# Kernel optimization log

Hardware: AMD Instinct MI355X
Metric: run time of the kernel (lower is better)

## Reference

```python
import jax, jax.numpy as jnp
import numpy as np
from jax import lax

# Key identity used: modulating ALL weights of output channel o by s_o (with no bias
# inside the modulated conv, as in the source where F.conv2d(..., bias=None)) is
# mathematically identical to a plain conv followed by per-(batch, out_channel)
# scaling of the output. This collapses the per-sample Python loop into one conv.

def _upsample2x(x):
    # nearest-neighbor x2, matching F.interpolate(scale_factor=2) default mode
    return jnp.repeat(jnp.repeat(x, 2, axis=2), 2, axis=3)

def _conv(x, w):
    return lax.conv_general_dilated(
        x, w, window_strides=(1, 1), padding=[(1, 1), (1, 1)],
        dimension_numbers=("NCHW", "OIHW", "NCHW"))

def _modconv(x, style, w, fc_w, fc_b):
    # style_fc: [B, style_dim] -> [B, out_ch]
    s = style @ fc_w.T + fc_b          # [B, O]
    y = _conv(x, w)                    # [B, O, H, W]
    return y * s[:, :, None, None]


def setup_inputs() -> dict:
    key = jax.random.key(0)
    ks = jax.random.split(key, 16)
    B, SD = 8, 512
    chans = [(512, 256), (256, 128), (128, 64), (64, 64), (64, 64)]
    inp = {
        "x": jax.random.normal(ks[0], (B, 512, 8, 8), jnp.float32),
        "style": jax.random.normal(ks[1], (B, SD), jnp.float32),
    }
    for i, (ci, co) in enumerate(chans, start=1):
        inp[f"w{i}"] = jax.random.normal(ks[2 * i], (co, ci, 3, 3), jnp.float32) * (1.0 / np.sqrt(ci * 9))
        inp[f"fw{i}"] = jax.random.normal(ks[2 * i + 1], (co, SD), jnp.float32) * (1.0 / np.sqrt(SD))
        inp[f"fb{i}"] = jnp.ones((co,), jnp.float32)
    inp["wf"] = jax.random.normal(ks[12], (3, 64, 3, 3), jnp.float32) * (1.0 / np.sqrt(64 * 9))
    inp["bf"] = jnp.zeros((3,), jnp.float32)
    return inp


def reference(x, style, w1, fw1, fb1, w2, fw2, fb2, w3, fw3, fb3,
              w4, fw4, fb4, w5, fw5, fb5, wf, bf):
    x = _upsample2x(x)
    x = jax.nn.relu(_modconv(x, style, w1, fw1, fb1))
    x = _upsample2x(x)
    x = jax.nn.relu(_modconv(x, style, w2, fw2, fb2))
    x = _upsample2x(x)
    x = jax.nn.relu(_modconv(x, style, w3, fw3, fb3))
    x = _upsample2x(x)
    x = jax.nn.relu(_modconv(x, style, w4, fw4, fb4))
    x = _upsample2x(x)
    x = jax.nn.relu(_modconv(x, style, w5, fw5, fb5))
    x = _conv(x, wf) + bf[None, :, None, None]
    return x
```

## Files before the change

kernel.cpp:

```cpp
#include <hip/hip_runtime.h>
#include <hip/hip_bf16.h>
#include <cstddef>

typedef __bf16 bf16x8 __attribute__((ext_vector_type(8)));
typedef float f32x4 __attribute__((ext_vector_type(4)));

__global__ void prep_all_kernel(const float* __restrict__ x, __hip_bfloat16* __restrict__ act0,
                                const float* __restrict__ w1, __hip_bfloat16* __restrict__ o1,
                                const float* __restrict__ w2, __hip_bfloat16* __restrict__ o2,
                                const float* __restrict__ w3, __hip_bfloat16* __restrict__ o3,
                                const float* __restrict__ w4, __hip_bfloat16* __restrict__ o4,
                                const float* __restrict__ w5, __hip_bfloat16* __restrict__ o5,
                                const float* __restrict__ wf, __hip_bfloat16* __restrict__ of,
                                const float* __restrict__ style,
                                const float* __restrict__ fw1, const float* __restrict__ fb1,
                                const float* __restrict__ fw2, const float* __restrict__ fb2,
                                const float* __restrict__ fw3, const float* __restrict__ fb3,
                                const float* __restrict__ fw4, const float* __restrict__ fb4,
                                const float* __restrict__ fw5, const float* __restrict__ fb5,
                                float* __restrict__ S) {
    const int blk = blockIdx.x;
    if (blk < 1024) {
        int t = blk * 256 + threadIdx.x;
        int c = t & 511; int rest = t >> 9;
        int w = rest & 7; rest >>= 3; int h = rest & 7; int b = rest >> 3;
        act0[t] = __float2bfloat16(x[((b * 512 + c) * 8 + h) * 8 + w]);
    } else if (blk < 12324) {
        int t = (blk - 1024) * 256 + threadIdx.x;
        if (t < 2752512) {
            const float* w; __hip_bfloat16* o; int CI, lgCICH, lgCO16;
            if      (t < 2097152) { w = w1; o = o1; CI = 512; lgCICH = 3; lgCO16 = 4; }
            else if (t < 2621440) { t -= 2097152; w = w2; o = o2; CI = 256; lgCICH = 2; lgCO16 = 3; }
            else                  { t -= 2621440; w = w3; o = o3; CI = 128; lgCICH = 1; lgCO16 = 2; }
            int j    = t & 7;
            int ln   = (t >> 3) & 63;
            int ch   = (t >> 9) & 1;
            int cich = (t >> 10) & ((1 << lgCICH) - 1);
            int co16 = (t >> (10 + lgCICH)) & ((1 << lgCO16) - 1);
            int tap  = (t >> (10 + lgCICH + lgCO16)) & 3;
            int cls  = (t >> (12 + lgCICH + lgCO16)) & 3;
            int co = co16 * 16 + (ln & 15);
            int ci = cich * 64 + ch * 32 + (ln >> 4) * 8 + j;
            int py = cls >> 1, px = cls & 1;
            int i = tap >> 1, jj = tap & 1;
            int r0 = i * (1 + py), rc = py ? (2 - i) : (1 + i);
            int c0 = jj * (1 + px), cc = px ? (2 - jj) : (1 + jj);
            const float* wb = w + ((size_t)co * CI + ci) * 9;
            float s = 0.f;
            for (int rr = 0; rr < rc; ++rr)
                for (int c2 = 0; c2 < cc; ++c2)
                    s += wb[(r0 + rr) * 3 + (c0 + c2)];
            o[t] = __float2bfloat16(s);
        } else if (t < 2883584) {
            int u = t - 2752512;
            const float* w; __hip_bfloat16* o;
            if (u < 65536) { w = w4; o = o4; }
            else           { u -= 65536; w = w5; o = o5; }
            int j   = u & 7;
            int ln  = (u >> 3) & 63;
            int ch  = (u >> 9) & 1;
            int nt  = (u >> 10) & 3;
            int tp  = (u >> 12) & 3;
            int cls = (u >> 14) & 3;
            int py = cls >> 1, px = cls & 1;
            int i = tp >> 1, jj = tp & 1;
            int co = nt * 16 + (ln & 15);
            int ci = ch * 32 + (ln >> 4) * 8 + j;
            int r0 = i * (1 + py), rc = py ? (2 - i) : (1 + i);
            int c0 = jj * (1 + px), cc = px ? (2 - jj) : (1 + jj);
            const float* wb = w + ((size_t)co * 64 + ci) * 9;
            float s = 0.f;
            for (int rr = 0; rr < rc; ++rr)
                for (int c2 = 0; c2 < cc; ++c2)
                    s += wb[(r0 + rr) * 3 + (c0 + c2)];
            o[u] = __float2bfloat16(s);
        } else if (t < 2892800) {
            int u = t - 2883584;
            int j  = u & 7;
            int ln = (u >> 3) & 63;
            int ch = (u >> 9) & 1;
            int tap = u >> 10;
            int rr = ln & 15, qq = ln >> 4;
            int pos = ch * 32 + qq * 8 + j;
            int ci = (pos & 3) * 16 + (pos >> 2);
            float v = (rr < 3) ? wf[((size_t)rr * 64 + ci) * 9 + tap] : 0.f;
            of[u] = __float2bfloat16(v);
        }
    } else {
        int wvid = (blk - 12324) * 4 + (threadIdx.x >> 6);
        int lane = threadIdx.x & 63;
        const float* fw; const float* fb; int lg, sOff, local;
        if      (wvid < 2048) { fw = fw1; fb = fb1; lg = 8; sOff = 0;    local = wvid; }
        else if (wvid < 3072) { fw = fw2; fb = fb2; lg = 7; sOff = 2048; local = wvid - 2048; }
        else if (wvid < 3584) { fw = fw3; fb = fb3; lg = 6; sOff = 3072; local = wvid - 3072; }
        else if (wvid < 4096) { fw = fw4; fb = fb4; lg = 6; sOff = 3584; local = wvid - 3584; }
        else                  { fw = fw5; fb = fb5; lg = 6; sOff = 4096; local = wvid - 4096; }
        int b = local >> lg, o = local & ((1 << lg) - 1);
        const float* sb = style + b * 512;
        const float* fwo = fw + (size_t)o * 512;
        float p = 0.f;
        #pragma unroll
        for (int k = lane; k < 512; k += 64) p += sb[k] * fwo[k];
        #pragma unroll
        for (int off = 32; off > 0; off >>= 1) p += __shfl_down(p, off);
        if (lane == 0) S[sOff + local] = p + fb[o];
    }
}

template <int HS, int CI, int CO, int NT>
__launch_bounds__(256)
__global__ void conv_sfull_kernel(const __hip_bfloat16* __restrict__ actIn,
                                  const __hip_bfloat16* __restrict__ wpk,
                                  const float* __restrict__ S,
                                  __hip_bfloat16* __restrict__ actOut) {
    constexpr int WS = HS, HO = HS * 2;
    constexpr int CICH = CI / 64, CO16 = CO / 16;
    constexpr int PW = HO / 8, PPI = PW * PW;

    const int tid = threadIdx.x;
    const int lane = tid & 63, wv = tid >> 6;
    const int r = lane & 15, q = lane >> 4;
    const int rr2 = r >> 2, cc2 = r & 3;
    const int lane8 = lane * 8;
    const int py = wv >> 1, px = wv & 1;

    const int b = blockIdx.x / PPI;
    const int prest = blockIdx.x - b * PPI;
    const int ph = prest / PW, pwi = prest - ph * PW;
    const int oh0 = ph * 8, ow0 = pwi * 8;
    const int sh0 = oh0 >> 1, sw0 = ow0 >> 1;
    const int co16base = blockIdx.y * NT;
    const int n0 = co16base * 16;

    __shared__ alignas(16) __hip_bfloat16 Tile[36 * 72];

    f32x4 acc[NT];
    #pragma unroll
    for (int j = 0; j < NT; ++j) acc[j] = f32x4{0.f, 0.f, 0.f, 0.f};

    bf16x8 bA[NT][2], bB[NT][2];

    #pragma unroll 1
    for (int cich = 0; cich < CICH; ++cich) {
        if (cich) __syncthreads();
        for (int i = tid; i < 288; i += 256) {
            int pix = i >> 3, koct = i & 7;
            int tr = pix / 6, tc2 = pix - tr * 6;
            int su = sh0 - 1 + tr, sv = sw0 - 1 + tc2;
            uint4 v = {0, 0, 0, 0};
            if (su >= 0 && su < HS && sv >= 0 && sv < WS)
                v = *(const uint4*)(actIn +
                    ((size_t)((b * HS + su) * WS + sv) * CI + cich * 64 + koct * 8));
            *(uint4*)&Tile[pix * 72 + koct * 8] = v;
        }
        __syncthreads();

        auto loadB = [&](bf16x8 (&dst)[NT][2], int tp) {
            #pragma unroll
            for (int nt = 0; nt < NT; ++nt)
                #pragma unroll
                for (int ch = 0; ch < 2; ++ch)
                    dst[nt][ch] = *(const bf16x8*)(wpk +
                        ((size_t)((((wv * 4 + tp) * CO16 + co16base + nt) * CICH + cich) * 2 + ch) << 9) + lane8);
        };

        auto compute = [&](int tp, bf16x8 (&bfr)[NT][2]) {
            const int i = tp >> 1, j = tp & 1;
            const int apix = (rr2 + i + py) * 6 + (cc2 + j + px);
            #pragma unroll
            for (int ch = 0; ch < 2; ++ch) {
                bf16x8 af = *(const bf16x8*)&Tile[apix * 72 + ch * 32 + q * 8];
                #pragma unroll
                for (int nt = 0; nt < NT; ++nt)
                    acc[nt] = __builtin_amdgcn_mfma_f32_16x16x32_bf16(
                        af, bfr[nt][ch], acc[nt], 0, 0, 0);
            }
        };

        loadB(bA, 0);
        loadB(bB, 1);
        compute(0, bA);
        loadB(bA, 2);
        compute(1, bB);
        loadB(bB, 3);
        compute(2, bA);
        compute(3, bB);
    }

    float sv_[NT];
    #pragma unroll
    for (int nt = 0; nt < NT; ++nt) sv_[nt] = S[b * CO + n0 + nt * 16 + r];
    #pragma unroll
    for (int t2 = 0; t2 < 4; ++t2) {
        const int m = q * 4 + t2;
        const int row = oh0 + 2 * (m >> 2) + py;
        const int col = ow0 + 2 * (m & 3) + px;
        const size_t obase = ((size_t)(b * HO + row) * HO + col) * CO + n0;
        #pragma unroll
        for (int nt = 0; nt < NT; ++nt)
            actOut[obase + nt * 16 + r] =
                __float2bfloat16(fmaxf(acc[nt][t2] * sv_[nt], 0.f));
    }
}

template <int HS, int WS>
__launch_bounds__(256)
__global__ void conv_patch_kernel(const __hip_bfloat16* __restrict__ actIn,
                                  const __hip_bfloat16* __restrict__ wpk,
                                  const float* __restrict__ S,
                                  __hip_bfloat16* __restrict__ actOut) {
    constexpr int HO = HS * 2, WO = WS * 2;

    const int tid = threadIdx.x;
    const int lane = tid & 63, wv = tid >> 6;
    const int r = lane & 15, q = lane >> 4;
    const int rs = r >> 3, sc = r & 7;
    const int lane8 = lane * 8;
    const int py = wv >> 1, px = wv & 1;

    const int pw = WO / 16, ppb = (HO / 16) * pw;
    const int b = blockIdx.x / ppb;
    const int prest = blockIdx.x - b * ppb;
    const int ph = prest / pw, pwi = prest - ph * pw;
    const int oh0 = ph * 16, ow0 = pwi * 16;
    const int sh0 = oh0 >> 1, sw0 = ow0 >> 1;

    __shared__ alignas(16) __hip_bfloat16 Tile[100 * 72];

    f32x4 acc[4][4];
    #pragma unroll
    for (int i = 0; i < 4; ++i)
        #pragma unroll
        for (int j = 0; j < 4; ++j) acc[i][j] = f32x4{0.f, 0.f, 0.f, 0.f};

    for (int i = tid; i < 800; i += 256) {
        int pix = i >> 3, koct = i & 7;
        int tr = pix / 10, tc2 = pix - tr * 10;
        int su = sh0 - 1 + tr, sv = sw0 - 1 + tc2;
        uint4 v = {0, 0, 0, 0};
        if (su >= 0 && su < HS && sv >= 0 && sv < WS)
            v = *(const uint4*)(actIn + ((size_t)((b * HS + su) * WS + sv) * 64 + koct * 8));
        *(uint4*)&Tile[pix * 72 + koct * 8] = v;
    }
    __syncthreads();

    const __hip_bfloat16* wcls = wpk + ((size_t)wv << 14);

    bf16x8 bA[4][2], bB[4][2];

    auto loadB = [&](bf16x8 (&dst)[4][2], int tp) {
        #pragma unroll
        for (int nt = 0; nt < 4; ++nt)
            #pragma unroll
            for (int ch = 0; ch < 2; ++ch)
                dst[nt][ch] = *(const bf16x8*)(wcls + (tp << 12) + ((nt * 2 + ch) << 9) + lane8);
    };

    auto compute = [&](int tp, bf16x8 (&bfr)[4][2]) {
        const int i = tp >> 1, j = tp & 1;
        const int ro = i + py, co2 = j + px;
        int apix[4];
        #pragma unroll
        for (int mt = 0; mt < 4; ++mt)
            apix[mt] = (2 * mt + rs + ro) * 10 + (sc + co2);
        #pragma unroll
        for (int ch = 0; ch < 2; ++ch) {
            bf16x8 af[4];
            #pragma unroll
            for (int mt = 0; mt < 4; ++mt)
                af[mt] = *(const bf16x8*)&Tile[apix[mt] * 72 + ch * 32 + q * 8];
            #pragma unroll
            for (int mt = 0; mt < 4; ++mt)
                #pragma unroll
                for (int nt = 0; nt < 4; ++nt)
                    acc[mt][nt] = __builtin_amdgcn_mfma_f32_16x16x32_bf16(
                        af[mt], bfr[nt][ch], acc[mt][nt], 0, 0, 0);
        }
    };

    loadB(bA, 0);
    loadB(bB, 1);
    compute(0, bA);
    loadB(bA, 2);
    compute(1, bB);
    loadB(bB, 3);
    compute(2, bA);
    compute(3, bB);

    float sv_[4];
    #pragma unroll
    for (int nt = 0; nt < 4; ++nt) sv_[nt] = S[b * 64 + nt * 16 + r];
    #pragma unroll
    for (int mt = 0; mt < 4; ++mt) {
        #pragma unroll
        for (int t2 = 0; t2 < 4; ++t2) {
            const int m = q * 4 + t2;
            const int row = oh0 + 4 * mt + 2 * (m >> 3) + py;
            const int col = ow0 + 2 * (m & 7) + px;
            const size_t obase = ((size_t)(b * HO + row) * WO + col) * 64;
            #pragma unroll
            for (int nt = 0; nt < 4; ++nt)
                actOut[obase + nt * 16 + r] =
                    __float2bfloat16(fmaxf(acc[mt][nt][t2] * sv_[nt], 0.f));
        }
    }
}

__launch_bounds__(512)
__global__ void conv_s5f_kernel(const __hip_bfloat16* __restrict__ actIn,
                                const __hip_bfloat16* __restrict__ wpk5,
                                const __hip_bfloat16* __restrict__ wpkF,
                                const float* __restrict__ S,
                                const float* __restrict__ bias,
                                float* __restrict__ out) {
    constexpr int HS = 128, WS = 128;

    const int tid = threadIdx.x;
    const int lane = tid & 63, wv = tid >> 6;
    const int r = lane & 15, q = lane >> 4;
    const int lane8 = lane * 8;
    const int cls = wv >> 1, half = wv & 1;
    const int py = cls >> 1, px = cls & 1;

    const int bid = blockIdx.x;
    const int b = bid >> 8;
    const int rest = bid & 255;
    const int oh0 = (rest >> 4) * 16, ow0 = (rest & 15) * 16;
    const int sh0 = oh0 >> 1, sw0 = ow0 >> 1;

    __shared__ alignas(16) __hip_bfloat16 Lds[18 * 18 * 72];
    __hip_bfloat16* TileA = Lds;

    for (int i = tid; i < 800; i += 512) {
        int pix = i >> 3, koct = i & 7;
        int tr = pix / 10, tc2 = pix - tr * 10;
        int su = sh0 - 1 + tr, sv = sw0 - 1 + tc2;
        uint4 v = {0, 0, 0, 0};
        if (su >= 0 && su < HS && sv >= 0 && sv < WS)
            v = *(const uint4*)(actIn + ((size_t)((b * HS + su) * WS + sv) * 64 + koct * 8));
        *(uint4*)&TileA[pix * 72 + koct * 8] = v;
    }
    __syncthreads();

    f32x4 acc[3][4];
    #pragma unroll
    for (int i = 0; i < 3; ++i)
        #pragma unroll
        for (int j = 0; j < 4; ++j) acc[i][j] = f32x4{0.f, 0.f, 0.f, 0.f};

    int jrA[3], jcA[3];
    #pragma unroll
    for (int mt = 0; mt < 3; ++mt) {
        int pm = half * 48 + mt * 16 + r;
        pm = pm > 80 ? 80 : pm;
        jrA[mt] = (pm * 57) >> 9;
        jcA[mt] = pm - jrA[mt] * 9;
    }

    const __hip_bfloat16* wcls = wpk5 + ((size_t)cls << 14);

    bf16x8 bA[4][2], bB[4][2];

    auto loadB = [&](bf16x8 (&dst)[4][2], int tp) {
        #pragma unroll
        for (int nt = 0; nt < 4; ++nt)
            #pragma unroll
            for (int ch = 0; ch < 2; ++ch)
                dst[nt][ch] = *(const bf16x8*)(wcls + (tp << 12) + ((nt * 2 + ch) << 9) + lane8);
    };

    auto compute = [&](int tp, bf16x8 (&bfr)[4][2]) {
        const int i = tp >> 1, j = tp & 1;
        int apix[3];
        #pragma unroll
        for (int mt = 0; mt < 3; ++mt)
            apix[mt] = (jrA[mt] + i) * 10 + (jcA[mt] + j);
        #pragma unroll
        for (int ch = 0; ch < 2; ++ch) {
            bf16x8 af[3];
            #pragma unroll
            for (int mt = 0; mt < 3; ++mt)
                af[mt] = *(const bf16x8*)&TileA[apix[mt] * 72 + ch * 32 + q * 8];
            #pragma unroll
            for (int mt = 0; mt < 3; ++mt)
                #pragma unroll
                for (int nt = 0; nt < 4; ++nt)
                    acc[mt][nt] = __builtin_amdgcn_mfma_f32_16x16x32_bf16(
                        af[mt], bfr[nt][ch], acc[mt][nt], 0, 0, 0);
        }
    };

    loadB(bA, 0);
    loadB(bB, 1);
    compute(0, bA);
    loadB(bA, 2);
    compute(1, bB);
    loadB(bB, 3);
    compute(2, bA);
    compute(3, bB);

    float sv_[4];
    #pragma unroll
    for (int nt = 0; nt < 4; ++nt) sv_[nt] = S[b * 64 + nt * 16 + r];

    __syncthreads();

    #pragma unroll
    for (int mt = 0; mt < 3; ++mt) {
        #pragma unroll
        for (int t2 = 0; t2 < 4; ++t2) {
            const int m = half * 48 + mt * 16 + q * 4 + t2;
            if (m < 81) {
                const int jr = (m * 57) >> 9;
                const int jc = m - jr * 9;
                const int p  = py ? (oh0 - 1 + 2 * jr) : (oh0 + 2 * jr);
                const int pc = px ? (ow0 - 1 + 2 * jc) : (ow0 + 2 * jc);
                const bool valid = (p >= 0) && (p < 256) && (pc >= 0) && (pc < 256);
                const int dpx = (2 * jr + 1 - py) * 18 + (2 * jc + 1 - px);
                union { ushort4 u; __hip_bfloat16 h[4]; } pk;
                #pragma unroll
                for (int nt = 0; nt < 4; ++nt) {
                    float v = valid ? fmaxf(acc[mt][nt][t2] * sv_[nt], 0.f) : 0.f;
                    pk.h[nt] = __float2bfloat16(v);
                }
                *(ushort4*)&Lds[dpx * 72 + r * 4] = pk.u;
            }
        }
    }
    __syncthreads();

    f32x4 acc2[2];
    acc2[0] = f32x4{0.f, 0.f, 0.f, 0.f};
    acc2[1] = f32x4{0.f, 0.f, 0.f, 0.f};

    #pragma unroll 1
    for (int tap = 0; tap < 9; ++tap) {
        const int dyv = tap / 3;
        const int dxv = tap - dyv * 3;
        const int tc = r + dxv;
        int apix[2];
        #pragma unroll
        for (int mt = 0; mt < 2; ++mt)
            apix[mt] = (wv * 2 + mt + dyv) * 18 + tc;
        #pragma unroll
        for (int ch = 0; ch < 2; ++ch) {
            bf16x8 bfr = *(const bf16x8*)(wpkF + ((tap * 2 + ch) << 9) + lane8);
            #pragma unroll
            for (int mt = 0; mt < 2; ++mt) {
                bf16x8 af = *(const bf16x8*)&Lds[apix[mt] * 72 + ch * 32 + q * 8];
                acc2[mt] = __builtin_amdgcn_mfma_f32_16x16x32_bf16(af, bfr, acc2[mt], 0, 0, 0);
            }
        }
    }

    if (r < 3) {
        const float bs = bias[r];
        #pragma unroll
        for (int mt = 0; mt < 2; ++mt) {
            const int prow = oh0 + wv * 2 + mt;
            #pragma unroll
            for (int t2 = 0; t2 < 4; ++t2)
                out[((size_t)(b * 3 + r) << 16) + prow * 256 + ow0 + q * 4 + t2] =
                    acc2[mt][t2] + bs;
        }
    }
}

extern "C" void kernel_launch(void* const* d_in, const int* in_sizes, int n_in,
                              void* d_out, int out_size, void* d_ws, size_t ws_size,
                              hipStream_t stream) {
    const float* x    = (const float*)d_in[0];
    const float* sty  = (const float*)d_in[1];
    const float* w1   = (const float*)d_in[2];
    const float* fw1  = (const float*)d_in[3];
    const float* fb1  = (const float*)d_in[4];
    const float* w2   = (const float*)d_in[5];
    const float* fw2  = (const float*)d_in[6];
    const float* fb2  = (const float*)d_in[7];
    const float* w3   = (const float*)d_in[8];
    const float* fw3  = (const float*)d_in[9];
    const float* fb3  = (const float*)d_in[10];
    const float* w4   = (const float*)d_in[11];
    const float* fw4  = (const float*)d_in[12];
    const float* fb4  = (const float*)d_in[13];
    const float* w5   = (const float*)d_in[14];
    const float* fw5  = (const float*)d_in[15];
    const float* fb5  = (const float*)d_in[16];
    const float* wf   = (const float*)d_in[17];
    const float* bf   = (const float*)d_in[18];
    float* out = (float*)d_out;

    char* ws = (char*)d_ws;
    size_t off = 0;
    auto alloc = [&](size_t bytes) {
        char* p = ws + off;
        off += (bytes + 255) & ~(size_t)255;
        return p;
    };
    float* S1 = (float*)alloc(8 * 256 * 4);
    float* S2 = (float*)alloc(8 * 128 * 4);
    float* S3 = (float*)alloc(8 * 64 * 4);
    float* S4 = (float*)alloc(8 * 64 * 4);
    float* S5 = (float*)alloc(8 * 64 * 4);
    __hip_bfloat16* act0 = (__hip_bfloat16*)alloc((size_t)262144 * 2);
    __hip_bfloat16* act1 = (__hip_bfloat16*)alloc((size_t)524288 * 2);
    __hip_bfloat16* act2 = (__hip_bfloat16*)alloc((size_t)1048576 * 2);
    __hip_bfloat16* act3 = (__hip_bfloat16*)alloc((size_t)2097152 * 2);
    __hip_bfloat16* act4 = (__hip_bfloat16*)alloc((size_t)8388608 * 2);
    __hip_bfloat16* wt1  = (__hip_bfloat16*)alloc((size_t)2097152 * 2);
    __hip_bfloat16* wt2  = (__hip_bfloat16*)alloc((size_t)524288 * 2);
    __hip_bfloat16* wt3  = (__hip_bfloat16*)alloc((size_t)131072 * 2);
    __hip_bfloat16* wt4  = (__hip_bfloat16*)alloc((size_t)65536 * 2);
    __hip_bfloat16* wt5  = (__hip_bfloat16*)alloc((size_t)65536 * 2);
    __hip_bfloat16* wtF  = (__hip_bfloat16*)alloc((size_t)9 * 16 * 64 * 2);
    if (off > ws_size) return;

    prep_all_kernel<<<13476, 256, 0, stream>>>(x, act0,
                                               w1, wt1, w2, wt2, w3, wt3,
                                               w4, wt4, w5, wt5, wf, wtF,
                                               sty, fw1, fb1, fw2, fb2, fw3, fb3,
                                               fw4, fb4, fw5, fb5, S1);

    conv_sfull_kernel<8, 512, 256, 1><<<dim3(32, 16), 256, 0, stream>>>(act0, wt1, S1, act1);
    conv_sfull_kernel<16, 256, 128, 2><<<dim3(128, 4), 256, 0, stream>>>(act1, wt2, S2, act2);
    conv_sfull_kernel<32, 128, 64, 4><<<dim3(512, 1), 256, 0, stream>>>(act2, wt3, S3, act3);

    conv_patch_kernel<64, 64><<<dim3(512), 256, 0, stream>>>(act3, wt4, S4, act4);

    conv_s5f_kernel<<<2048, 512, 0, stream>>>(act4, wt5, wtF, S5, bf, out);
}
```

Baseline: 194.0 us.

## Fuse stage-4 conv into stage-5/final kernel, recomputing stage-4 tiles with halo

Layer 4's upsample-conv is folded into the combined layer-5 and final-conv kernel. Each block loads a 7x7 stage-3 patch, computes the 10x10 stage-4 tile with its halo in LDS, then runs layers 5 and final as before. This drops the 16 MB act4 write and read round trip and one kernel launch. In exchange, the halo regions of layer 4 are recomputed in neighbouring blocks, and each block uses more LDS. The layer-5 weight packing now permutes input channels to match the LDS layout that the fused stage writes.

```diff
diff --git a/kernel.cpp b/kernel.cpp
--- a/kernel.cpp
+++ b/kernel.cpp
@@ -53,9 +53,9 @@
             o[t] = __float2bfloat16(s);
         } else if (t < 2883584) {
             int u = t - 2752512;
-            const float* w; __hip_bfloat16* o;
-            if (u < 65536) { w = w4; o = o4; }
-            else           { u -= 65536; w = w5; o = o5; }
+            const float* w; __hip_bfloat16* o; bool perm;
+            if (u < 65536) { w = w4; o = o4; perm = false; }
+            else           { u -= 65536; w = w5; o = o5; perm = true; }
             int j   = u & 7;
             int ln  = (u >> 3) & 63;
             int ch  = (u >> 9) & 1;
@@ -65,7 +65,8 @@
             int py = cls >> 1, px = cls & 1;
             int i = tp >> 1, jj = tp & 1;
             int co = nt * 16 + (ln & 15);
-            int ci = ch * 32 + (ln >> 4) * 8 + j;
+            int pos = ch * 32 + (ln >> 4) * 8 + j;
+            int ci = perm ? ((pos & 3) * 16 + (pos >> 2)) : pos;
             int r0 = i * (1 + py), rc = py ? (2 - i) : (1 + i);
             int c0 = jj * (1 + px), cc = px ? (2 - jj) : (1 + jj);
             const float* wb = w + ((size_t)co * 64 + ci) * 9;
@@ -203,49 +204,125 @@
     }
 }
 
-template <int HS, int WS>
-__launch_bounds__(256)
-__global__ void conv_patch_kernel(const __hip_bfloat16* __restrict__ actIn,
-                                  const __hip_bfloat16* __restrict__ wpk,
-                                  const float* __restrict__ S,
-                                  __hip_bfloat16* __restrict__ actOut) {
-    constexpr int HO = HS * 2, WO = WS * 2;
-
+__launch_bounds__(512)
+__global__ void conv_s45f_kernel(const __hip_bfloat16* __restrict__ actIn,
+                                 const __hip_bfloat16* __restrict__ wpk4,
+                                 const __hip_bfloat16* __restrict__ wpk5,
+                                 const __hip_bfloat16* __restrict__ wpkF,
+                                 const float* __restrict__ S4,
+                                 const float* __restrict__ S5,
+                                 const float* __restrict__ bias,
+                                 float* __restrict__ out) {
     const int tid = threadIdx.x;
     const int lane = tid & 63, wv = tid >> 6;
     const int r = lane & 15, q = lane >> 4;
-    const int rs = r >> 3, sc = r & 7;
     const int lane8 = lane * 8;
-    const int py = wv >> 1, px = wv & 1;
-
-    const int pw = WO / 16, ppb = (HO / 16) * pw;
-    const int b = blockIdx.x / ppb;
-    const int prest = blockIdx.x - b * ppb;
-    const int ph = prest / pw, pwi = prest - ph * pw;
-    const int oh0 = ph * 16, ow0 = pwi * 16;
+    const int cls = wv >> 1, half = wv & 1;
+    const int py = cls >> 1, px = cls & 1;
+
+    const int bid = blockIdx.x;
+    const int b = bid >> 8;
+    const int rest = bid & 255;
+    const int oh0 = (rest >> 4) * 16, ow0 = (rest & 15) * 16;
     const int sh0 = oh0 >> 1, sw0 = ow0 >> 1;
-
-    __shared__ alignas(16) __hip_bfloat16 Tile[100 * 72];
-
-    f32x4 acc[4][4];
-    #pragma unroll
-    for (int i = 0; i < 4; ++i)
+    const int s3h0 = oh0 >> 2, s3w0 = ow0 >> 2;
+
+    __shared__ alignas(16) __hip_bfloat16 A4[10 * 10 * 72];
+    __shared__ alignas(16) __hip_bfloat16 A5[18 * 18 * 72];
+    __hip_bfloat16* A3 = A5;
+
+    for (int i = tid; i < 392; i += 512) {
+        int pix = i >> 3, koct = i & 7;
+        int tr = pix / 7, tc = pix - tr * 7;
+        int su = s3h0 - 1 + tr, sv = s3w0 - 1 + tc;
+        uint4 v = {0, 0, 0, 0};
+        if (su >= 0 && su < 64 && sv >= 0 && sv < 64)
+            v = *(const uint4*)(actIn + ((size_t)((b * 64 + su) * 64 + sv) * 64 + koct * 8));
+        *(uint4*)&A3[pix * 72 + koct * 8] = v;
+    }
+    __syncthreads();
+
+    {
+        f32x4 acc4[4];
+        #pragma unroll
+        for (int j = 0; j < 4; ++j) acc4[j] = f32x4{0.f, 0.f, 0.f, 0.f};
+
+        int cpA = half * 16 + r; if (cpA > 24) cpA = 24;
+        const int ua = (cpA * 205) >> 10, va = cpA - ua * 5;
+
+        const __hip_bfloat16* w4c = wpk4 + ((size_t)cls << 14);
+        bf16x8 b4A[4][2], b4B[4][2];
+
+        auto loadB4 = [&](bf16x8 (&dst)[4][2], int tp) {
+            #pragma unroll
+            for (int nt = 0; nt < 4; ++nt)
+                #pragma unroll
+                for (int ch = 0; ch < 2; ++ch)
+                    dst[nt][ch] = *(const bf16x8*)(w4c + (tp << 12) + ((nt * 2 + ch) << 9) + lane8);
+        };
+        auto compute4 = [&](int tp, bf16x8 (&bfr)[4][2]) {
+            const int i = tp >> 1, j = tp & 1;
+            const int apix = (ua + i) * 7 + (va + j);
+            #pragma unroll
+            for (int ch = 0; ch < 2; ++ch) {
+                bf16x8 af = *(const bf16x8*)&A3[apix * 72 + ch * 32 + q * 8];
+                #pragma unroll
+                for (int nt = 0; nt < 4; ++nt)
+                    acc4[nt] = __builtin_amdgcn_mfma_f32_16x16x32_bf16(
+                        af, bfr[nt][ch], acc4[nt], 0, 0, 0);
+            }
+        };
+
+        loadB4(b4A, 0);
+        loadB4(b4B, 1);
+        compute4(0, b4A);
+        loadB4(b4A, 2);
+        compute4(1, b4B);
+        loadB4(b4B, 3);
+        compute4(2, b4A);
+        compute4(3, b4B);
+
+        float sv4[4];
+        #pragma unroll
+        for (int nt = 0; nt < 4; ++nt) sv4[nt] = S4[b * 64 + nt * 16 + r];
+
+        #pragma unroll
+        for (int t2 = 0; t2 < 4; ++t2) {
+            const int cp = half * 16 + q * 4 + t2;
+            if (cp < 25) {
+                const int uu = (cp * 205) >> 10, vv = cp - uu * 5;
+                const int a4r = sh0 - py + 2 * uu;
+                const int a4c = sw0 - px + 2 * vv;
+                const bool valid = (a4r >= 0) && (a4r < 128) && (a4c >= 0) && (a4c < 128);
+                const int dpx = (2 * uu + 1 - py) * 10 + (2 * vv + 1 - px);
+                union { ushort4 u4; __hip_bfloat16 h[4]; } pk;
+                #pragma unroll
+                for (int nt = 0; nt < 4; ++nt) {
+                    float v = valid ? fmaxf(acc4[nt][t2] * sv4[nt], 0.f) : 0.f;
+                    pk.h[nt] = __float2bfloat16(v);
+                }
+                *(ushort4*)&A4[dpx * 72 + r * 4] = pk.u4;
+            }
+        }
+    }
+    __syncthreads();
+
+    f32x4 acc[3][4];
+    #pragma unroll
+    for (int i = 0; i < 3; ++i)
         #pragma unroll
         for (int j = 0; j < 4; ++j) acc[i][j] = f32x4{0.f, 0.f, 0.f, 0.f};
 
-    for (int i = tid; i < 800; i += 256) {
-        int pix = i >> 3, koct = i & 7;
-        int tr = pix / 10, tc2 = pix - tr * 10;
-        int su = sh0 - 1 + tr, sv = sw0 - 1 + tc2;
-        uint4 v = {0, 0, 0, 0};
-        if (su >= 0 && su < HS && sv >= 0 && sv < WS)
-            v = *(const uint4*)(actIn + ((size_t)((b * HS + su) * WS + sv) * 64 + koct * 8));
-        *(uint4*)&Tile[pix * 72 + koct * 8] = v;
-    }
-    __syncthreads();
-
-    const __hip_bfloat16* wcls = wpk + ((size_t)wv << 14);
-
+    int jrA[3], jcA[3];
+    #pragma unroll
+    for (int mt = 0; mt < 3; ++mt) {
+        int pm = half * 48 + mt * 16 + r;
+        pm = pm > 80 ? 80 : pm;
+        jrA[mt] = (pm * 57) >> 9;
+        jcA[mt] = pm - jrA[mt] * 9;
+    }
+
+    const __hip_bfloat16* wcls = wpk5 + ((size_t)cls << 14);
     bf16x8 bA[4][2], bB[4][2];
 
     auto loadB = [&](bf16x8 (&dst)[4][2], int tp) {
@@ -255,22 +332,20 @@
             for (int ch = 0; ch < 2; ++ch)
                 dst[nt][ch] = *(const bf16x8*)(wcls + (tp << 12) + ((nt * 2 + ch) << 9) + lane8);
     };
-
     auto compute = [&](int tp, bf16x8 (&bfr)[4][2]) {
         const int i = tp >> 1, j = tp & 1;
-        const int ro = i + py, co2 = j + px;
-        int apix[4];
-        #pragma unroll
-        for (int mt = 0; mt < 4; ++mt)
-            apix[mt] = (2 * mt + rs + ro) * 10 + (sc + co2);
+        int apix[3];
+        #pragma unroll
+        for (int mt = 0; mt < 3; ++mt)
+            apix[mt] = (jrA[mt] + i) * 10 + (jcA[mt] + j);
         #pragma unroll
         for (int ch = 0; ch < 2; ++ch) {
-            bf16x8 af[4];
-            #pragma unroll
-            for (int mt = 0; mt < 4; ++mt)
-                af[mt] = *(const bf16x8*)&Tile[apix[mt] * 72 + ch * 32 + q * 8];
-            #pragma unroll
-            for (int mt = 0; mt < 4; ++mt)
+            bf16x8 af[3];
+            #pragma unroll
+            for (int mt = 0; mt < 3; ++mt)
+                af[mt] = *(const bf16x8*)&A4[apix[mt] * 72 + ch * 32 + q * 8];
+            #pragma unroll
+            for (int mt = 0; mt < 3; ++mt)
                 #pragma unroll
                 for (int nt = 0; nt < 4; ++nt)
                     acc[mt][nt] = __builtin_amdgcn_mfma_f32_16x16x32_bf16(
@@ -289,121 +364,7 @@
 
     float sv_[4];
     #pragma unroll
-    for (int nt = 0; nt < 4; ++nt) sv_[nt] = S[b * 64 + nt * 16 + r];
-    #pragma unroll
-    for (int mt = 0; mt < 4; ++mt) {
-        #pragma unroll
-        for (int t2 = 0; t2 < 4; ++t2) {
-            const int m = q * 4 + t2;
-            const int row = oh0 + 4 * mt + 2 * (m >> 3) + py;
-            const int col = ow0 + 2 * (m & 7) + px;
-            const size_t obase = ((size_t)(b * HO + row) * WO + col) * 64;
-            #pragma unroll
-            for (int nt = 0; nt < 4; ++nt)
-                actOut[obase + nt * 16 + r] =
-                    __float2bfloat16(fmaxf(acc[mt][nt][t2] * sv_[nt], 0.f));
-        }
-    }
-}
-
-__launch_bounds__(512)
-__global__ void conv_s5f_kernel(const __hip_bfloat16* __restrict__ actIn,
-                                const __hip_bfloat16* __restrict__ wpk5,
-                                const __hip_bfloat16* __restrict__ wpkF,
-                                const float* __restrict__ S,
-                                const float* __restrict__ bias,
-                                float* __restrict__ out) {
-    constexpr int HS = 128, WS = 128;
-
-    const int tid = threadIdx.x;
-    const int lane = tid & 63, wv = tid >> 6;
-    const int r = lane & 15, q = lane >> 4;
-    const int lane8 = lane * 8;
-    const int cls = wv >> 1, half = wv & 1;
-    const int py = cls >> 1, px = cls & 1;
-
-    const int bid = blockIdx.x;
-    const int b = bid >> 8;
-    const int rest = bid & 255;
-    const int oh0 = (rest >> 4) * 16, ow0 = (rest & 15) * 16;
-    const int sh0 = oh0 >> 1, sw0 = ow0 >> 1;
-
-    __shared__ alignas(16) __hip_bfloat16 Lds[18 * 18 * 72];
-    __hip_bfloat16* TileA = Lds;
-
-    for (int i = tid; i < 800; i += 512) {
-        int pix = i >> 3, koct = i & 7;
-        int tr = pix / 10, tc2 = pix - tr * 10;
-        int su = sh0 - 1 + tr, sv = sw0 - 1 + tc2;
-        uint4 v = {0, 0, 0, 0};
-        if (su >= 0 && su < HS && sv >= 0 && sv < WS)
-            v = *(const uint4*)(actIn + ((size_t)((b * HS + su) * WS + sv) * 64 + koct * 8));
-        *(uint4*)&TileA[pix * 72 + koct * 8] = v;
-    }
-    __syncthreads();
-
-    f32x4 acc[3][4];
-    #pragma unroll
-    for (int i = 0; i < 3; ++i)
-        #pragma unroll
-        for (int j = 0; j < 4; ++j) acc[i][j] = f32x4{0.f, 0.f, 0.f, 0.f};
-
-    int jrA[3], jcA[3];
-    #pragma unroll
-    for (int mt = 0; mt < 3; ++mt) {
-        int pm = half * 48 + mt * 16 + r;
-        pm = pm > 80 ? 80 : pm;
-        jrA[mt] = (pm * 57) >> 9;
-        jcA[mt] = pm - jrA[mt] * 9;
-    }
-
-    const __hip_bfloat16* wcls = wpk5 + ((size_t)cls << 14);
-
-    bf16x8 bA[4][2], bB[4][2];
-
-    auto loadB = [&](bf16x8 (&dst)[4][2], int tp) {
-        #pragma unroll
-        for (int nt = 0; nt < 4; ++nt)
-            #pragma unroll
-            for (int ch = 0; ch < 2; ++ch)
-                dst[nt][ch] = *(const bf16x8*)(wcls + (tp << 12) + ((nt * 2 + ch) << 9) + lane8);
-    };
-
-    auto compute = [&](int tp, bf16x8 (&bfr)[4][2]) {
-        const int i = tp >> 1, j = tp & 1;
-        int apix[3];
-        #pragma unroll
-        for (int mt = 0; mt < 3; ++mt)
-            apix[mt] = (jrA[mt] + i) * 10 + (jcA[mt] + j);
-        #pragma unroll
-        for (int ch = 0; ch < 2; ++ch) {
-            bf16x8 af[3];
-            #pragma unroll
-            for (int mt = 0; mt < 3; ++mt)
-                af[mt] = *(const bf16x8*)&TileA[apix[mt] * 72 + ch * 32 + q * 8];
-            #pragma unroll
-            for (int mt = 0; mt < 3; ++mt)
-                #pragma unroll
-                for (int nt = 0; nt < 4; ++nt)
-                    acc[mt][nt] = __builtin_amdgcn_mfma_f32_16x16x32_bf16(
-                        af[mt], bfr[nt][ch], acc[mt][nt], 0, 0, 0);
-        }
-    };
-
-    loadB(bA, 0);
-    loadB(bB, 1);
-    compute(0, bA);
-    loadB(bA, 2);
-    compute(1, bB);
-    loadB(bB, 3);
-    compute(2, bA);
-    compute(3, bB);
-
-    float sv_[4];
-    #pragma unroll
-    for (int nt = 0; nt < 4; ++nt) sv_[nt] = S[b * 64 + nt * 16 + r];
-
-    __syncthreads();
+    for (int nt = 0; nt < 4; ++nt) sv_[nt] = S5[b * 64 + nt * 16 + r];
 
     #pragma unroll
     for (int mt = 0; mt < 3; ++mt) {
@@ -417,13 +378,13 @@
                 const int pc = px ? (ow0 - 1 + 2 * jc) : (ow0 + 2 * jc);
                 const bool valid = (p >= 0) && (p < 256) && (pc >= 0) && (pc < 256);
                 const int dpx = (2 * jr + 1 - py) * 18 + (2 * jc + 1 - px);
-                union { ushort4 u; __hip_bfloat16 h[4]; } pk;
+                union { ushort4 u4; __hip_bfloat16 h[4]; } pk;
                 #pragma unroll
                 for (int nt = 0; nt < 4; ++nt) {
                     float v = valid ? fmaxf(acc[mt][nt][t2] * sv_[nt], 0.f) : 0.f;
                     pk.h[nt] = __float2bfloat16(v);
                 }
-                *(ushort4*)&Lds[dpx * 72 + r * 4] = pk.u;
+                *(ushort4*)&A5[dpx * 72 + r * 4] = pk.u4;
             }
         }
     }
@@ -447,7 +408,7 @@
             bf16x8 bfr = *(const bf16x8*)(wpkF + ((tap * 2 + ch) << 9) + lane8);
             #pragma unroll
             for (int mt = 0; mt < 2; ++mt) {
-                bf16x8 af = *(const bf16x8*)&Lds[apix[mt] * 72 + ch * 32 + q * 8];
+                bf16x8 af = *(const bf16x8*)&A5[apix[mt] * 72 + ch * 32 + q * 8];
                 acc2[mt] = __builtin_amdgcn_mfma_f32_16x16x32_bf16(af, bfr, acc2[mt], 0, 0, 0);
             }
         }
@@ -506,7 +467,6 @@
     __hip_bfloat16* act1 = (__hip_bfloat16*)alloc((size_t)524288 * 2);
     __hip_bfloat16* act2 = (__hip_bfloat16*)alloc((size_t)1048576 * 2);
     __hip_bfloat16* act3 = (__hip_bfloat16*)alloc((size_t)2097152 * 2);
-    __hip_bfloat16* act4 = (__hip_bfloat16*)alloc((size_t)8388608 * 2);
     __hip_bfloat16* wt1  = (__hip_bfloat16*)alloc((size_t)2097152 * 2);
     __hip_bfloat16* wt2  = (__hip_bfloat16*)alloc((size_t)524288 * 2);
     __hip_bfloat16* wt3  = (__hip_bfloat16*)alloc((size_t)131072 * 2);
@@ -525,7 +485,5 @@
     conv_sfull_kernel<16, 256, 128, 2><<<dim3(128, 4), 256, 0, stream>>>(act1, wt2, S2, act2);
     conv_sfull_kernel<32, 128, 64, 4><<<dim3(512, 1), 256, 0, stream>>>(act2, wt3, S3, act3);
 
-    conv_patch_kernel<64, 64><<<dim3(512), 256, 0, stream>>>(act3, wt4, S4, act4);
-
-    conv_s5f_kernel<<<2048, 512, 0, stream>>>(act4, wt5, wtF, S5, bf, out);
+    conv_s45f_kernel<<<2048, 512, 0, stream>>>(act3, wt4, wt5, wtF, S4, S5, bf, out);
 }
```

Measured after the change: 200.1 us. 3.2% more time.
